# Kernel optimization log

Measured on AMD Instinct MI355X. Metric: run time of the kernel, lower is better.

## Reference

```python
import jax, jax.numpy as jnp
import numpy as np

QUANT_BLOCK = 32  # hardcoded in Linear8Bit


def setup_inputs() -> dict:
    key = jax.random.key(0)
    k1, k2, k3, k4, k5 = jax.random.split(key, 5)
    M, K, N = 64, 8192, 8192
    num_blocks = K // QUANT_BLOCK  # 256
    x = jax.random.normal(k1, (M, K), dtype=jnp.float32)
    scales = jax.random.uniform(k2, (num_blocks, N), dtype=jnp.float32, minval=0.001, maxval=0.02)
    zeros = jax.random.uniform(k3, (num_blocks, N), dtype=jnp.float32, minval=0.0, maxval=255.0)
    bias = jax.random.normal(k4, (N,), dtype=jnp.float32)
    quantized_weight = jax.random.randint(k5, (K, N), 0, 256, dtype=jnp.int32)
    return {"x": x, "scales": scales, "zeros": zeros, "bias": bias,
            "quantized_weight": quantized_weight}


def reference(x, scales, zeros, bias, quantized_weight):
    # The torch loop computes sum_b a_block @ (scale_b * (w_block - zero_b)),
    # which is exactly a full block-wise dequant followed by one matmul.
    K, N = quantized_weight.shape
    # Expand per-block scale/zero along K: [num_blocks, N] -> [K, N]
    scale_k = jnp.repeat(scales, QUANT_BLOCK, axis=0)[:K]
    zero_k = jnp.repeat(zeros, QUANT_BLOCK, axis=0)[:K]
    w_dq = scale_k * (quantized_weight.astype(jnp.float32) - zero_k)  # [K, N]
    out = jnp.matmul(x, w_dq) + bias  # [M, N]
    return out
```

## Files before the change

kernel.cpp:

```cpp
#include <hip/hip_runtime.h>

#define M_DIM 64
#define K_DIM 8192
#define N_DIM 8192
#define QB 32
#define NT 64
#define KC 64
#define SPLITS 4
#define KSPLIT (K_DIM / SPLITS)
#define NSTAGE (KSPLIT / KC)

typedef __attribute__((ext_vector_type(8))) short short8;
typedef __attribute__((ext_vector_type(8))) unsigned short ushort8;
typedef __attribute__((ext_vector_type(4))) float f32x4;

static_assert(NSTAGE * KC == KSPLIT, "split must tile");

__device__ __forceinline__ unsigned short f2bf(float f) {
    unsigned u = __builtin_bit_cast(unsigned, f);
    u += 0x7fffu + ((u >> 16) & 1u);
    return (unsigned short)(u >> 16);
}

__global__ __launch_bounds__(256) void bias_init(const float* __restrict__ bias,
                                                 float* __restrict__ out) {
    int i = (blockIdx.x * 256 + threadIdx.x) * 4;
    int n = i & (N_DIM - 1);
    *(f32x4*)(out + i) = *(const f32x4*)(bias + n);
}

__global__ __launch_bounds__(256, 2) void qgemm(
    const float* __restrict__ x,
    const float* __restrict__ scales,
    const float* __restrict__ zeros,
    const int*   __restrict__ qw,
    float*       __restrict__ out)
{
    __shared__ unsigned short lq[2][NT][72];
    __shared__ unsigned short lx[2][M_DIM][72];

    const int tid  = threadIdx.x;
    const int lane = tid & 63;
    const int w    = tid >> 6;

    const int n0 = blockIdx.x * NT;
    const int k0 = blockIdx.y * KSPLIT;

    const int qn   = n0 + lane;
    const int xrow = tid >> 2;
    const int xcol = (tid & 3) * 16;

    int   qv[16];
    float sv0, sv1, zv0, zv1;
    f32x4 xv[4];

    auto load_stage = [&](int kk) {
        #pragma unroll
        for (int s = 0; s < 4; ++s)
            #pragma unroll
            for (int j = 0; j < 4; ++j)
                qv[s * 4 + j] = qw[(size_t)(kk + 16 * s + 4 * w + j) * N_DIM + qn];
        const int b0 = kk >> 5;
        sv0 = scales[(size_t)b0 * N_DIM + qn];
        sv1 = scales[(size_t)(b0 + 1) * N_DIM + qn];
        zv0 = zeros[(size_t)b0 * N_DIM + qn];
        zv1 = zeros[(size_t)(b0 + 1) * N_DIM + qn];
        #pragma unroll
        for (int i = 0; i < 4; ++i)
            xv[i] = *(const f32x4*)(x + (size_t)xrow * K_DIM + kk + xcol + 4 * i);
    };

    load_stage(k0);

    f32x4 acc[4];
    #pragma unroll
    for (int r = 0; r < 4; ++r) acc[r] = (f32x4){0.f, 0.f, 0.f, 0.f};

    for (int t = 0; t < NSTAGE; ++t) {
        const int cur = t & 1;

        const float nz0 = -sv0 * zv0, nz1 = -sv1 * zv1;
        const float s0r = sv0, s1r = sv1;
        uint2 qd[4];
        #pragma unroll
        for (int s = 0; s < 4; ++s) {
            const float sc = (s < 2) ? s0r : s1r;
            const float nz = (s < 2) ? nz0 : nz1;
            unsigned short h0 = f2bf(fmaf((float)qv[s * 4 + 0], sc, nz));
            unsigned short h1 = f2bf(fmaf((float)qv[s * 4 + 1], sc, nz));
            unsigned short h2 = f2bf(fmaf((float)qv[s * 4 + 2], sc, nz));
            unsigned short h3 = f2bf(fmaf((float)qv[s * 4 + 3], sc, nz));
            qd[s].x = (unsigned)h0 | ((unsigned)h1 << 16);
            qd[s].y = (unsigned)h2 | ((unsigned)h3 << 16);
        }
        ushort8 xw0, xw1;
        #pragma unroll
        for (int e = 0; e < 4; ++e) {
            xw0[e]     = f2bf(xv[0][e]);
            xw0[4 + e] = f2bf(xv[1][e]);
            xw1[e]     = f2bf(xv[2][e]);
            xw1[4 + e] = f2bf(xv[3][e]);
        }

        if (t + 1 < NSTAGE) load_stage(k0 + (t + 1) * KC);

        #pragma unroll
        for (int s = 0; s < 4; ++s)
            *(uint2*)&lq[cur][lane][16 * s + 4 * w] = qd[s];
        *(ushort8*)&lx[cur][xrow][xcol]     = xw0;
        *(ushort8*)&lx[cur][xrow][xcol + 8] = xw1;

        __syncthreads();

        #pragma unroll
        for (int c = 0; c < 2; ++c) {
            const short8 bf = *(const short8*)&lq[cur][16 * w + (lane & 15)]
                                                [32 * c + 8 * (lane >> 4)];
            #pragma unroll
            for (int r = 0; r < 4; ++r) {
                const short8 af = *(const short8*)&lx[cur][16 * r + (lane & 15)]
                                                    [32 * c + 8 * (lane >> 4)];
                acc[r] = __builtin_amdgcn_mfma_f32_16x16x32_bf16(af, bf, acc[r], 0, 0, 0);
            }
        }
    }

    const int cn = n0 + 16 * w + (lane & 15);
    #pragma unroll
    for (int r = 0; r < 4; ++r) {
        const int m = 16 * r + 4 * (lane >> 4);
        #pragma unroll
        for (int e = 0; e < 4; ++e)
            atomicAdd(out + (size_t)(m + e) * N_DIM + cn, acc[r][e]);
    }
}

extern "C" void kernel_launch(void* const* d_in, const int* in_sizes, int n_in,
                              void* d_out, int out_size, void* d_ws, size_t ws_size,
                              hipStream_t stream) {
    const float* x      = (const float*)d_in[0];
    const float* scales = (const float*)d_in[1];
    const float* zeros  = (const float*)d_in[2];
    const float* bias   = (const float*)d_in[3];
    const int*   qw     = (const int*)d_in[4];
    float* out = (float*)d_out;

    bias_init<<<dim3((M_DIM * N_DIM) / 1024), 256, 0, stream>>>(bias, out);
    qgemm<<<dim3(N_DIM / NT, SPLITS), 256, 0, stream>>>(x, scales, zeros, qw, out);
}
```

Before: 60.24 us.

## Per-wave K-slab dequant, pre-convert x to bf16, drop block sync, double splits

Each wave now dequantizes its own 16 columns across a full 64-wide K chunk in a private LDS tile, which removes the block-wide __syncthreads and the shared x tile. A separate kernel converts x to bf16 once into workspace, and the A fragments are read straight from global memory. Split-K goes from 4 to 8, the launch bound asks for 4 blocks per CU, and the int32 weights are read with nontemporal loads. The intent is more parallelism, fewer barriers and less repeated x conversion. The cost is an extra launch, twice as many output atomics, and redundant global reads of x that now rely on the cache.

```diff
diff --git a/kernel.cpp b/kernel.cpp
--- a/kernel.cpp
+++ b/kernel.cpp
@@ -6,13 +6,14 @@
 #define QB 32
 #define NT 64
 #define KC 64
-#define SPLITS 4
+#define SPLITS 8
 #define KSPLIT (K_DIM / SPLITS)
 #define NSTAGE (KSPLIT / KC)
 
 typedef __attribute__((ext_vector_type(8))) short short8;
 typedef __attribute__((ext_vector_type(8))) unsigned short ushort8;
 typedef __attribute__((ext_vector_type(4))) float f32x4;
+typedef __attribute__((ext_vector_type(4))) unsigned int u32x4;
 
 static_assert(NSTAGE * KC == KSPLIT, "split must tile");
 
@@ -25,113 +26,124 @@
 __global__ __launch_bounds__(256) void bias_init(const float* __restrict__ bias,
                                                  float* __restrict__ out) {
     int i = (blockIdx.x * 256 + threadIdx.x) * 4;
-    int n = i & (N_DIM - 1);
-    *(f32x4*)(out + i) = *(const f32x4*)(bias + n);
+    *(f32x4*)(out + i) = *(const f32x4*)(bias + (i & (N_DIM - 1)));
 }
 
-__global__ __launch_bounds__(256, 2) void qgemm(
+__global__ __launch_bounds__(256) void xcvt(const float* __restrict__ x,
+                                            unsigned short* __restrict__ xb) {
+    int i = (blockIdx.x * 256 + threadIdx.x) * 8;
+    f32x4 a = *(const f32x4*)(x + i);
+    f32x4 b = *(const f32x4*)(x + i + 4);
+    ushort8 o;
+    #pragma unroll
+    for (int e = 0; e < 4; ++e) { o[e] = f2bf(a[e]); o[4 + e] = f2bf(b[e]); }
+    *(ushort8*)(xb + i) = o;
+}
+
+template <bool XBF>
+__global__ __launch_bounds__(256, 4) void qgemm(
     const float* __restrict__ x,
+    const unsigned short* __restrict__ xb,
     const float* __restrict__ scales,
     const float* __restrict__ zeros,
     const int*   __restrict__ qw,
     float*       __restrict__ out)
 {
-    __shared__ unsigned short lq[2][NT][72];
-    __shared__ unsigned short lx[2][M_DIM][72];
+    __shared__ unsigned short lq[4][16][72];
 
     const int tid  = threadIdx.x;
     const int lane = tid & 63;
     const int w    = tid >> 6;
+    const int lr   = lane & 15;
+    const int q    = lane >> 4;
 
-    const int n0 = blockIdx.x * NT;
-    const int k0 = blockIdx.y * KSPLIT;
+    const int n0  = blockIdx.x * NT;
+    const int k0  = blockIdx.y * KSPLIT;
+    const int col = n0 + 16 * w + lr;
 
-    const int qn   = n0 + lane;
-    const int xrow = tid >> 2;
-    const int xcol = (tid & 3) * 16;
+    const int*   qp = qw     + (size_t)(k0 + 16 * q) * N_DIM + col;
+    const float* sp = scales + (size_t)((k0 >> 5) + (q >> 1)) * N_DIM + col;
+    const float* zp = zeros  + (size_t)((k0 >> 5) + (q >> 1)) * N_DIM + col;
 
-    int   qv[16];
-    float sv0, sv1, zv0, zv1;
-    f32x4 xv[4];
-
-    auto load_stage = [&](int kk) {
-        #pragma unroll
-        for (int s = 0; s < 4; ++s)
-            #pragma unroll
-            for (int j = 0; j < 4; ++j)
-                qv[s * 4 + j] = qw[(size_t)(kk + 16 * s + 4 * w + j) * N_DIM + qn];
-        const int b0 = kk >> 5;
-        sv0 = scales[(size_t)b0 * N_DIM + qn];
-        sv1 = scales[(size_t)(b0 + 1) * N_DIM + qn];
-        zv0 = zeros[(size_t)b0 * N_DIM + qn];
-        zv1 = zeros[(size_t)(b0 + 1) * N_DIM + qn];
-        #pragma unroll
-        for (int i = 0; i < 4; ++i)
-            xv[i] = *(const f32x4*)(x + (size_t)xrow * K_DIM + kk + xcol + 4 * i);
-    };
-
-    load_stage(k0);
+    int qv[16];
+    #pragma unroll
+    for (int j = 0; j < 16; ++j)
+        qv[j] = __builtin_nontemporal_load(qp + (size_t)j * N_DIM);
+    float sv = __builtin_nontemporal_load(sp);
+    float zv = __builtin_nontemporal_load(zp);
 
     f32x4 acc[4];
     #pragma unroll
     for (int r = 0; r < 4; ++r) acc[r] = (f32x4){0.f, 0.f, 0.f, 0.f};
 
     for (int t = 0; t < NSTAGE; ++t) {
-        const int cur = t & 1;
+        const int kk = k0 + t * KC;
 
-        const float nz0 = -sv0 * zv0, nz1 = -sv1 * zv1;
-        const float s0r = sv0, s1r = sv1;
-        uint2 qd[4];
-        #pragma unroll
-        for (int s = 0; s < 4; ++s) {
-            const float sc = (s < 2) ? s0r : s1r;
-            const float nz = (s < 2) ? nz0 : nz1;
-            unsigned short h0 = f2bf(fmaf((float)qv[s * 4 + 0], sc, nz));
-            unsigned short h1 = f2bf(fmaf((float)qv[s * 4 + 1], sc, nz));
-            unsigned short h2 = f2bf(fmaf((float)qv[s * 4 + 2], sc, nz));
-            unsigned short h3 = f2bf(fmaf((float)qv[s * 4 + 3], sc, nz));
-            qd[s].x = (unsigned)h0 | ((unsigned)h1 << 16);
-            qd[s].y = (unsigned)h2 | ((unsigned)h3 << 16);
-        }
-        ushort8 xw0, xw1;
-        #pragma unroll
-        for (int e = 0; e < 4; ++e) {
-            xw0[e]     = f2bf(xv[0][e]);
-            xw0[4 + e] = f2bf(xv[1][e]);
-            xw1[e]     = f2bf(xv[2][e]);
-            xw1[4 + e] = f2bf(xv[3][e]);
+        short8 af[4][2];
+        if (XBF) {
+            const unsigned short* xp = xb + (size_t)lr * K_DIM + kk + 8 * q;
+            #pragma unroll
+            for (int r = 0; r < 4; ++r)
+                #pragma unroll
+                for (int c = 0; c < 2; ++c)
+                    af[r][c] = *(const short8*)(xp + (size_t)r * 16 * K_DIM + 32 * c);
+        } else {
+            #pragma unroll
+            for (int r = 0; r < 4; ++r)
+                #pragma unroll
+                for (int c = 0; c < 2; ++c) {
+                    const float* xp = x + (size_t)(16 * r + lr) * K_DIM + kk + 32 * c + 8 * q;
+                    f32x4 u = *(const f32x4*)xp;
+                    f32x4 v = *(const f32x4*)(xp + 4);
+                    #pragma unroll
+                    for (int e = 0; e < 4; ++e) {
+                        af[r][c][e]     = (short)f2bf(u[e]);
+                        af[r][c][4 + e] = (short)f2bf(v[e]);
+                    }
+                }
         }
 
-        if (t + 1 < NSTAGE) load_stage(k0 + (t + 1) * KC);
+        const float nz = -sv * zv;
+        const float sc = sv;
+        unsigned hh[8];
+        #pragma unroll
+        for (int j = 0; j < 8; ++j) {
+            unsigned short h0 = f2bf(fmaf((float)qv[2 * j],     sc, nz));
+            unsigned short h1 = f2bf(fmaf((float)qv[2 * j + 1], sc, nz));
+            hh[j] = (unsigned)h0 | ((unsigned)h1 << 16);
+        }
+
+        if (t + 1 < NSTAGE) {
+            qp += (size_t)KC * N_DIM;
+            #pragma unroll
+            for (int j = 0; j < 16; ++j)
+                qv[j] = __builtin_nontemporal_load(qp + (size_t)j * N_DIM);
+            sp += 2 * N_DIM; zp += 2 * N_DIM;
+            sv = __builtin_nontemporal_load(sp);
+            zv = __builtin_nontemporal_load(zp);
+        }
+
+        *(u32x4*)&lq[w][lr][16 * q]     = (u32x4){hh[0], hh[1], hh[2], hh[3]};
+        *(u32x4*)&lq[w][lr][16 * q + 8] = (u32x4){hh[4], hh[5], hh[6], hh[7]};
+
+        short8 bf[2];
+        #pragma unroll
+        for (int c = 0; c < 2; ++c)
+            bf[c] = *(const short8*)&lq[w][lr][32 * c + 8 * q];
 
         #pragma unroll
-        for (int s = 0; s < 4; ++s)
-            *(uint2*)&lq[cur][lane][16 * s + 4 * w] = qd[s];
-        *(ushort8*)&lx[cur][xrow][xcol]     = xw0;
-        *(ushort8*)&lx[cur][xrow][xcol + 8] = xw1;
-
-        __syncthreads();
-
-        #pragma unroll
-        for (int c = 0; c < 2; ++c) {
-            const short8 bf = *(const short8*)&lq[cur][16 * w + (lane & 15)]
-                                                [32 * c + 8 * (lane >> 4)];
+        for (int c = 0; c < 2; ++c)
             #pragma unroll
-            for (int r = 0; r < 4; ++r) {
-                const short8 af = *(const short8*)&lx[cur][16 * r + (lane & 15)]
-                                                    [32 * c + 8 * (lane >> 4)];
-                acc[r] = __builtin_amdgcn_mfma_f32_16x16x32_bf16(af, bf, acc[r], 0, 0, 0);
-            }
-        }
+            for (int r = 0; r < 4; ++r)
+                acc[r] = __builtin_amdgcn_mfma_f32_16x16x32_bf16(af[r][c], bf[c], acc[r], 0, 0, 0);
     }
 
-    const int cn = n0 + 16 * w + (lane & 15);
     #pragma unroll
     for (int r = 0; r < 4; ++r) {
-        const int m = 16 * r + 4 * (lane >> 4);
+        const int m = 16 * r + 4 * q;
         #pragma unroll
         for (int e = 0; e < 4; ++e)
-            atomicAdd(out + (size_t)(m + e) * N_DIM + cn, acc[r][e]);
+            atomicAdd(out + (size_t)(m + e) * N_DIM + col, acc[r][e]);
     }
 }
 
@@ -144,7 +156,15 @@
     const float* bias   = (const float*)d_in[3];
     const int*   qw     = (const int*)d_in[4];
     float* out = (float*)d_out;
+    unsigned short* xbf = (unsigned short*)d_ws;
+
+    const bool use_xbf = ws_size >= (size_t)M_DIM * K_DIM * 2;
 
     bias_init<<<dim3((M_DIM * N_DIM) / 1024), 256, 0, stream>>>(bias, out);
-    qgemm<<<dim3(N_DIM / NT, SPLITS), 256, 0, stream>>>(x, scales, zeros, qw, out);
+    if (use_xbf) {
+        xcvt<<<dim3((M_DIM * K_DIM) / 2048), 256, 0, stream>>>(x, xbf);
+        qgemm<true><<<dim3(N_DIM / NT, SPLITS), 256, 0, stream>>>(x, xbf, scales, zeros, qw, out);
+    } else {
+        qgemm<false><<<dim3(N_DIM / NT, SPLITS), 256, 0, stream>>>(x, nullptr, scales, zeros, qw, out);
+    }
 }
```

New measurement: 114.7 us. 1.9x slower.

## Widen N tile to 256 with vectorized int4 weight loads and more K splits

Applied to the files above, without the earlier changes.

Restructures the quantized GEMM so each block covers 256 output columns with one 32-row K stage (a single quant block). Each lane now loads four adjacent weight columns with 128-bit loads, plus one scale and one zero vector per stage. Shared memory is laid out as K by N, and each wave computes a 64x64 output tile with 16 accumulators. This gives more MFMA work per x fragment and fewer, wider global loads. K is split 16 ways to keep the grid at 512 blocks, which quadruples the output atomics. The B fragments are gathered with strided scalar LDS reads, which can cause bank conflicts and more LDS instructions.

```diff
diff --git a/kernel.cpp b/kernel.cpp
--- a/kernel.cpp
+++ b/kernel.cpp
@@ -4,17 +4,18 @@
 #define K_DIM 8192
 #define N_DIM 8192
 #define QB 32
-#define NT 64
-#define KC 64
-#define SPLITS 4
+#define NT 256
+#define KC 32
+#define SPLITS 16
 #define KSPLIT (K_DIM / SPLITS)
 #define NSTAGE (KSPLIT / KC)
 
 typedef __attribute__((ext_vector_type(8))) short short8;
 typedef __attribute__((ext_vector_type(8))) unsigned short ushort8;
 typedef __attribute__((ext_vector_type(4))) float f32x4;
+typedef __attribute__((ext_vector_type(4))) int i32x4;
 
-static_assert(NSTAGE * KC == KSPLIT, "split must tile");
+static_assert(NSTAGE * KC == KSPLIT, "tiling");
 
 __device__ __forceinline__ unsigned short f2bf(float f) {
     unsigned u = __builtin_bit_cast(unsigned, f);
@@ -25,8 +26,7 @@
 __global__ __launch_bounds__(256) void bias_init(const float* __restrict__ bias,
                                                  float* __restrict__ out) {
     int i = (blockIdx.x * 256 + threadIdx.x) * 4;
-    int n = i & (N_DIM - 1);
-    *(f32x4*)(out + i) = *(const f32x4*)(bias + n);
+    *(f32x4*)(out + i) = *(const f32x4*)(bias + (i & (N_DIM - 1)));
 }
 
 __global__ __launch_bounds__(256, 2) void qgemm(
@@ -36,102 +36,106 @@
     const int*   __restrict__ qw,
     float*       __restrict__ out)
 {
-    __shared__ unsigned short lq[2][NT][72];
-    __shared__ unsigned short lx[2][M_DIM][72];
+    __shared__ unsigned short lw[2][KC][260];
+    __shared__ unsigned short lx[2][M_DIM][40];
 
     const int tid  = threadIdx.x;
     const int lane = tid & 63;
     const int w    = tid >> 6;
+    const int q    = lane >> 4;
+    const int lm   = lane & 15;
 
     const int n0 = blockIdx.x * NT;
     const int k0 = blockIdx.y * KSPLIT;
 
-    const int qn   = n0 + lane;
-    const int xrow = tid >> 2;
-    const int xcol = (tid & 3) * 16;
+    const int*   qbase = qw     + (size_t)k0 * N_DIM        + n0 + 4 * lane;
+    const float* sbase = scales + (size_t)(k0 >> 5) * N_DIM + n0 + 4 * lane;
+    const float* zbase = zeros  + (size_t)(k0 >> 5) * N_DIM + n0 + 4 * lane;
+    const float* xbase = x + (size_t)(tid >> 2) * K_DIM + k0 + (tid & 3) * 8;
 
-    int   qv[16];
-    float sv0, sv1, zv0, zv1;
-    f32x4 xv[4];
+    i32x4 qv[8];
+    f32x4 sc, zc, xv0, xv1;
 
-    auto load_stage = [&](int kk) {
+    auto load_stage = [&](int t) {
+        const int* p = qbase + (size_t)t * KC * N_DIM;
         #pragma unroll
-        for (int s = 0; s < 4; ++s)
-            #pragma unroll
-            for (int j = 0; j < 4; ++j)
-                qv[s * 4 + j] = qw[(size_t)(kk + 16 * s + 4 * w + j) * N_DIM + qn];
-        const int b0 = kk >> 5;
-        sv0 = scales[(size_t)b0 * N_DIM + qn];
-        sv1 = scales[(size_t)(b0 + 1) * N_DIM + qn];
-        zv0 = zeros[(size_t)b0 * N_DIM + qn];
-        zv1 = zeros[(size_t)(b0 + 1) * N_DIM + qn];
-        #pragma unroll
-        for (int i = 0; i < 4; ++i)
-            xv[i] = *(const f32x4*)(x + (size_t)xrow * K_DIM + kk + xcol + 4 * i);
+        for (int i = 0; i < 8; ++i)
+            qv[i] = *(const i32x4*)(p + (size_t)(4 * i + w) * N_DIM);
+        sc = *(const f32x4*)(sbase + (size_t)t * N_DIM);
+        zc = *(const f32x4*)(zbase + (size_t)t * N_DIM);
+        const float* xp = xbase + t * KC;
+        xv0 = *(const f32x4*)xp;
+        xv1 = *(const f32x4*)(xp + 4);
     };
 
-    load_stage(k0);
+    load_stage(0);
 
-    f32x4 acc[4];
+    f32x4 acc[4][4];
     #pragma unroll
-    for (int r = 0; r < 4; ++r) acc[r] = (f32x4){0.f, 0.f, 0.f, 0.f};
+    for (int a = 0; a < 4; ++a)
+        #pragma unroll
+        for (int b = 0; b < 4; ++b) acc[a][b] = (f32x4){0.f, 0.f, 0.f, 0.f};
 
     for (int t = 0; t < NSTAGE; ++t) {
         const int cur = t & 1;
 
-        const float nz0 = -sv0 * zv0, nz1 = -sv1 * zv1;
-        const float s0r = sv0, s1r = sv1;
-        uint2 qd[4];
+        const f32x4 nz = -sc * zc;
+        uint2 qd[8];
         #pragma unroll
-        for (int s = 0; s < 4; ++s) {
-            const float sc = (s < 2) ? s0r : s1r;
-            const float nz = (s < 2) ? nz0 : nz1;
-            unsigned short h0 = f2bf(fmaf((float)qv[s * 4 + 0], sc, nz));
-            unsigned short h1 = f2bf(fmaf((float)qv[s * 4 + 1], sc, nz));
-            unsigned short h2 = f2bf(fmaf((float)qv[s * 4 + 2], sc, nz));
-            unsigned short h3 = f2bf(fmaf((float)qv[s * 4 + 3], sc, nz));
-            qd[s].x = (unsigned)h0 | ((unsigned)h1 << 16);
-            qd[s].y = (unsigned)h2 | ((unsigned)h3 << 16);
+        for (int i = 0; i < 8; ++i) {
+            unsigned short h0 = f2bf(fmaf((float)qv[i][0], sc[0], nz[0]));
+            unsigned short h1 = f2bf(fmaf((float)qv[i][1], sc[1], nz[1]));
+            unsigned short h2 = f2bf(fmaf((float)qv[i][2], sc[2], nz[2]));
+            unsigned short h3 = f2bf(fmaf((float)qv[i][3], sc[3], nz[3]));
+            qd[i].x = (unsigned)h0 | ((unsigned)h1 << 16);
+            qd[i].y = (unsigned)h2 | ((unsigned)h3 << 16);
         }
-        ushort8 xw0, xw1;
+        ushort8 xw;
         #pragma unroll
         for (int e = 0; e < 4; ++e) {
-            xw0[e]     = f2bf(xv[0][e]);
-            xw0[4 + e] = f2bf(xv[1][e]);
-            xw1[e]     = f2bf(xv[2][e]);
-            xw1[4 + e] = f2bf(xv[3][e]);
+            xw[e]     = f2bf(xv0[e]);
+            xw[4 + e] = f2bf(xv1[e]);
         }
 
-        if (t + 1 < NSTAGE) load_stage(k0 + (t + 1) * KC);
+        if (t + 1 < NSTAGE) load_stage(t + 1);
 
         #pragma unroll
-        for (int s = 0; s < 4; ++s)
-            *(uint2*)&lq[cur][lane][16 * s + 4 * w] = qd[s];
-        *(ushort8*)&lx[cur][xrow][xcol]     = xw0;
-        *(ushort8*)&lx[cur][xrow][xcol + 8] = xw1;
+        for (int i = 0; i < 8; ++i)
+            *(uint2*)&lw[cur][4 * i + w][4 * lane] = qd[i];
+        *(ushort8*)&lx[cur][tid >> 2][(tid & 3) * 8] = xw;
 
         __syncthreads();
 
+        short8 bf[4];
         #pragma unroll
-        for (int c = 0; c < 2; ++c) {
-            const short8 bf = *(const short8*)&lq[cur][16 * w + (lane & 15)]
-                                                [32 * c + 8 * (lane >> 4)];
+        for (int g = 0; g < 4; ++g)
             #pragma unroll
-            for (int r = 0; r < 4; ++r) {
-                const short8 af = *(const short8*)&lx[cur][16 * r + (lane & 15)]
-                                                    [32 * c + 8 * (lane >> 4)];
-                acc[r] = __builtin_amdgcn_mfma_f32_16x16x32_bf16(af, bf, acc[r], 0, 0, 0);
-            }
-        }
+            for (int j = 0; j < 8; ++j)
+                bf[g][j] = (short)lw[cur][8 * q + j][64 * w + 16 * g + lm];
+
+        short8 af[4];
+        #pragma unroll
+        for (int rf = 0; rf < 4; ++rf)
+            af[rf] = *(const short8*)&lx[cur][16 * rf + lm][8 * q];
+
+        #pragma unroll
+        for (int g = 0; g < 4; ++g)
+            #pragma unroll
+            for (int rf = 0; rf < 4; ++rf)
+                acc[g][rf] = __builtin_amdgcn_mfma_f32_16x16x32_bf16(
+                    af[rf], bf[g], acc[g][rf], 0, 0, 0);
     }
 
-    const int cn = n0 + 16 * w + (lane & 15);
     #pragma unroll
-    for (int r = 0; r < 4; ++r) {
-        const int m = 16 * r + 4 * (lane >> 4);
+    for (int g = 0; g < 4; ++g) {
+        const int cn = n0 + 64 * w + 16 * g + lm;
         #pragma unroll
-        for (int e = 0; e < 4; ++e)
-            atomicAdd(out + (size_t)(m + e) * N_DIM + cn, acc[r][e]);
+        for (int rf = 0; rf < 4; ++rf) {
+            const int m = 16 * rf + 4 * q;
+            #pragma unroll
+            for (int e = 0; e < 4; ++e)
+                atomicAdd(out + (size_t)(m + e) * N_DIM + cn, acc[g][rf][e]);
+        }
     }
 }
 
```

Result: slower. 77.11 us (+28.0%).

## Pre-convert x to bf16 in workspace and double-buffer register prefetch across stages

Applied to the files above, without the earlier changes.

Adds a separate kernel that converts x to bf16 once into the workspace, so each GEMM block loads half as many x bytes and skips the per-block conversion. The main loop is unrolled by two with two register sets (A/B), issuing the next stage's global loads before the current stage's dequantisation, LDS stores and MFMAs. This is meant to hide global-load latency better and cut redundant x traffic and conversion work. In exchange it adds a kernel launch and roughly doubles the registers held for in-flight loads, which may lower occupancy under the two-blocks-per-CU launch bound.

```diff
diff --git a/kernel.cpp b/kernel.cpp
--- a/kernel.cpp
+++ b/kernel.cpp
@@ -13,8 +13,9 @@
 typedef __attribute__((ext_vector_type(8))) short short8;
 typedef __attribute__((ext_vector_type(8))) unsigned short ushort8;
 typedef __attribute__((ext_vector_type(4))) float f32x4;
-
-static_assert(NSTAGE * KC == KSPLIT, "split must tile");
+typedef __attribute__((ext_vector_type(4))) unsigned int u32x4;
+
+static_assert(NSTAGE % 2 == 0 && NSTAGE * KC == KSPLIT, "tiling");
 
 __device__ __forceinline__ unsigned short f2bf(float f) {
     unsigned u = __builtin_bit_cast(unsigned, f);
@@ -25,12 +26,24 @@
 __global__ __launch_bounds__(256) void bias_init(const float* __restrict__ bias,
                                                  float* __restrict__ out) {
     int i = (blockIdx.x * 256 + threadIdx.x) * 4;
-    int n = i & (N_DIM - 1);
-    *(f32x4*)(out + i) = *(const f32x4*)(bias + n);
-}
-
+    *(f32x4*)(out + i) = *(const f32x4*)(bias + (i & (N_DIM - 1)));
+}
+
+__global__ __launch_bounds__(256) void xcvt(const float* __restrict__ x,
+                                            unsigned short* __restrict__ xb) {
+    int i = (blockIdx.x * 256 + threadIdx.x) * 8;
+    f32x4 a = *(const f32x4*)(x + i);
+    f32x4 b = *(const f32x4*)(x + i + 4);
+    ushort8 o;
+    #pragma unroll
+    for (int e = 0; e < 4; ++e) { o[e] = f2bf(a[e]); o[4 + e] = f2bf(b[e]); }
+    *(ushort8*)(xb + i) = o;
+}
+
+template <bool XBF>
 __global__ __launch_bounds__(256, 2) void qgemm(
     const float* __restrict__ x,
+    const unsigned short* __restrict__ xb,
     const float* __restrict__ scales,
     const float* __restrict__ zeros,
     const int*   __restrict__ qw,
@@ -50,80 +63,111 @@
     const int xrow = tid >> 2;
     const int xcol = (tid & 3) * 16;
 
-    int   qv[16];
-    float sv0, sv1, zv0, zv1;
-    f32x4 xv[4];
-
-    auto load_stage = [&](int kk) {
-        #pragma unroll
-        for (int s = 0; s < 4; ++s)
-            #pragma unroll
-            for (int j = 0; j < 4; ++j)
-                qv[s * 4 + j] = qw[(size_t)(kk + 16 * s + 4 * w + j) * N_DIM + qn];
-        const int b0 = kk >> 5;
-        sv0 = scales[(size_t)b0 * N_DIM + qn];
-        sv1 = scales[(size_t)(b0 + 1) * N_DIM + qn];
-        zv0 = zeros[(size_t)b0 * N_DIM + qn];
-        zv1 = zeros[(size_t)(b0 + 1) * N_DIM + qn];
-        #pragma unroll
-        for (int i = 0; i < 4; ++i)
-            xv[i] = *(const f32x4*)(x + (size_t)xrow * K_DIM + kk + xcol + 4 * i);
-    };
-
-    load_stage(k0);
+    const int*   qp = qw     + (size_t)k0 * N_DIM + qn;
+    const float* sp = scales + (size_t)(k0 >> 5) * N_DIM + qn;
+    const float* zp = zeros  + (size_t)(k0 >> 5) * N_DIM + qn;
+
+    int   qvA[16], qvB[16];
+    float svA0, svA1, zvA0, zvA1, svB0, svB1, zvB0, zvB1;
+    u32x4 xvA[2], xvB[2];
+    f32x4 xfA[4], xfB[4];
+
+#define LOADS(QV, S0, S1, Z0, Z1, XV, XF, T)                                  \
+    do {                                                                      \
+        const int* _p = qp + (size_t)(T) * KC * N_DIM;                        \
+        _Pragma("unroll")                                                     \
+        for (int s = 0; s < 4; ++s)                                           \
+            _Pragma("unroll")                                                 \
+            for (int j = 0; j < 4; ++j)                                       \
+                QV[4 * s + j] = _p[(size_t)(16 * s + 4 * w + j) * N_DIM];     \
+        S0 = sp[(size_t)(2 * (T)) * N_DIM];                                   \
+        S1 = sp[(size_t)(2 * (T) + 1) * N_DIM];                               \
+        Z0 = zp[(size_t)(2 * (T)) * N_DIM];                                   \
+        Z1 = zp[(size_t)(2 * (T) + 1) * N_DIM];                               \
+        if (XBF) {                                                            \
+            const unsigned short* _xp =                                       \
+                xb + (size_t)xrow * K_DIM + (k0 + (T) * KC) + xcol;           \
+            XV[0] = *(const u32x4*)_xp;                                       \
+            XV[1] = *(const u32x4*)(_xp + 8);                                 \
+        } else {                                                              \
+            const float* _xp =                                                \
+                x + (size_t)xrow * K_DIM + (k0 + (T) * KC) + xcol;            \
+            _Pragma("unroll")                                                 \
+            for (int i = 0; i < 4; ++i) XF[i] = *(const f32x4*)(_xp + 4 * i); \
+        }                                                                     \
+    } while (0)
+
+#define BODY(QV, S0, S1, Z0, Z1, XV, XF, CUR)                                 \
+    do {                                                                      \
+        const float _nz0 = -(S0) * (Z0), _nz1 = -(S1) * (Z1);                 \
+        uint2 qd[4];                                                          \
+        _Pragma("unroll")                                                     \
+        for (int s = 0; s < 4; ++s) {                                         \
+            const float _sc = (s < 2) ? (S0) : (S1);                          \
+            const float _nz = (s < 2) ? _nz0 : _nz1;                          \
+            unsigned short h0 = f2bf(fmaf((float)QV[4 * s + 0], _sc, _nz));   \
+            unsigned short h1 = f2bf(fmaf((float)QV[4 * s + 1], _sc, _nz));   \
+            unsigned short h2 = f2bf(fmaf((float)QV[4 * s + 2], _sc, _nz));   \
+            unsigned short h3 = f2bf(fmaf((float)QV[4 * s + 3], _sc, _nz));   \
+            qd[s].x = (unsigned)h0 | ((unsigned)h1 << 16);                    \
+            qd[s].y = (unsigned)h2 | ((unsigned)h3 << 16);                    \
+        }                                                                     \
+        _Pragma("unroll")                                                     \
+        for (int s = 0; s < 4; ++s)                                           \
+            *(uint2*)&lq[CUR][lane][16 * s + 4 * w] = qd[s];                  \
+        if (XBF) {                                                            \
+            *(u32x4*)&lx[CUR][xrow][xcol]     = XV[0];                        \
+            *(u32x4*)&lx[CUR][xrow][xcol + 8] = XV[1];                        \
+        } else {                                                              \
+            ushort8 xw0, xw1;                                                 \
+            _Pragma("unroll")                                                 \
+            for (int e = 0; e < 4; ++e) {                                     \
+                xw0[e]     = f2bf(XF[0][e]);                                  \
+                xw0[4 + e] = f2bf(XF[1][e]);                                  \
+                xw1[e]     = f2bf(XF[2][e]);                                  \
+                xw1[4 + e] = f2bf(XF[3][e]);                                  \
+            }                                                                 \
+            *(ushort8*)&lx[CUR][xrow][xcol]     = xw0;                        \
+            *(ushort8*)&lx[CUR][xrow][xcol + 8] = xw1;                        \
+        }                                                                     \
+    } while (0)
+
+#define MM(CUR)                                                               \
+    do {                                                                      \
+        _Pragma("unroll")                                                     \
+        for (int c = 0; c < 2; ++c) {                                         \
+            const short8 bf = *(const short8*)&lq[CUR][16 * w + (lane & 15)]  \
+                                                 [32 * c + 8 * (lane >> 4)];  \
+            _Pragma("unroll")                                                 \
+            for (int r = 0; r < 4; ++r) {                                     \
+                const short8 af = *(const short8*)&lx[CUR][16 * r + (lane & 15)] \
+                                                     [32 * c + 8 * (lane >> 4)]; \
+                acc[r] = __builtin_amdgcn_mfma_f32_16x16x32_bf16(af, bf, acc[r], 0, 0, 0); \
+            }                                                                 \
+        }                                                                     \
+    } while (0)
 
     f32x4 acc[4];
     #pragma unroll
     for (int r = 0; r < 4; ++r) acc[r] = (f32x4){0.f, 0.f, 0.f, 0.f};
 
-    for (int t = 0; t < NSTAGE; ++t) {
-        const int cur = t & 1;
-
-        const float nz0 = -sv0 * zv0, nz1 = -sv1 * zv1;
-        const float s0r = sv0, s1r = sv1;
-        uint2 qd[4];
-        #pragma unroll
-        for (int s = 0; s < 4; ++s) {
-            const float sc = (s < 2) ? s0r : s1r;
-            const float nz = (s < 2) ? nz0 : nz1;
-            unsigned short h0 = f2bf(fmaf((float)qv[s * 4 + 0], sc, nz));
-            unsigned short h1 = f2bf(fmaf((float)qv[s * 4 + 1], sc, nz));
-            unsigned short h2 = f2bf(fmaf((float)qv[s * 4 + 2], sc, nz));
-            unsigned short h3 = f2bf(fmaf((float)qv[s * 4 + 3], sc, nz));
-            qd[s].x = (unsigned)h0 | ((unsigned)h1 << 16);
-            qd[s].y = (unsigned)h2 | ((unsigned)h3 << 16);
-        }
-        ushort8 xw0, xw1;
-        #pragma unroll
-        for (int e = 0; e < 4; ++e) {
-            xw0[e]     = f2bf(xv[0][e]);
-            xw0[4 + e] = f2bf(xv[1][e]);
-            xw1[e]     = f2bf(xv[2][e]);
-            xw1[4 + e] = f2bf(xv[3][e]);
-        }
-
-        if (t + 1 < NSTAGE) load_stage(k0 + (t + 1) * KC);
-
-        #pragma unroll
-        for (int s = 0; s < 4; ++s)
-            *(uint2*)&lq[cur][lane][16 * s + 4 * w] = qd[s];
-        *(ushort8*)&lx[cur][xrow][xcol]     = xw0;
-        *(ushort8*)&lx[cur][xrow][xcol + 8] = xw1;
-
+    LOADS(qvA, svA0, svA1, zvA0, zvA1, xvA, xfA, 0);
+
+    for (int t = 0; t < NSTAGE; t += 2) {
+        LOADS(qvB, svB0, svB1, zvB0, zvB1, xvB, xfB, t + 1);
+        BODY(qvA, svA0, svA1, zvA0, zvA1, xvA, xfA, 0);
         __syncthreads();
-
-        #pragma unroll
-        for (int c = 0; c < 2; ++c) {
-            const short8 bf = *(const short8*)&lq[cur][16 * w + (lane & 15)]
-                                                [32 * c + 8 * (lane >> 4)];
-            #pragma unroll
-            for (int r = 0; r < 4; ++r) {
-                const short8 af = *(const short8*)&lx[cur][16 * r + (lane & 15)]
-                                                    [32 * c + 8 * (lane >> 4)];
-                acc[r] = __builtin_amdgcn_mfma_f32_16x16x32_bf16(af, bf, acc[r], 0, 0, 0);
-            }
-        }
+        MM(0);
+        if (t + 2 < NSTAGE)
+            LOADS(qvA, svA0, svA1, zvA0, zvA1, xvA, xfA, t + 2);
+        BODY(qvB, svB0, svB1, zvB0, zvB1, xvB, xfB, 1);
+        __syncthreads();
+        MM(1);
     }
+
+#undef LOADS
+#undef BODY
+#undef MM
 
     const int cn = n0 + 16 * w + (lane & 15);
     #pragma unroll
@@ -144,7 +188,17 @@
     const float* bias   = (const float*)d_in[3];
     const int*   qw     = (const int*)d_in[4];
     float* out = (float*)d_out;
+    unsigned short* xbf = (unsigned short*)d_ws;
+
+    const bool use_xbf = ws_size >= (size_t)M_DIM * K_DIM * 2;
 
     bias_init<<<dim3((M_DIM * N_DIM) / 1024), 256, 0, stream>>>(bias, out);
-    qgemm<<<dim3(N_DIM / NT, SPLITS), 256, 0, stream>>>(x, scales, zeros, qw, out);
-}
+    if (use_xbf) {
+        xcvt<<<dim3((M_DIM * K_DIM) / 2048), 256, 0, stream>>>(x, xbf);
+        qgemm<true><<<dim3(N_DIM / NT, SPLITS), 256, 0, stream>>>(
+            x, xbf, scales, zeros, qw, out);
+    } else {
+        qgemm<false><<<dim3(N_DIM / NT, SPLITS), 256, 0, stream>>>(
+            x, nullptr, scales, zeros, qw, out);
+    }
+}
```

After: 59.91 us. Within noise of the previous version (-0.6%).
